# Kernel tuning notes

Hardware: AMD Instinct MI355X
Metric: run time of the kernel (lower is better)

Reference implementation:

```python
import jax, jax.numpy as jnp
import numpy as np

VOCAB = 1_000_000
EMBED = 128
NUM_NEG = 64
BATCH = 16384


def setup_inputs() -> dict:
    key = jax.random.key(0)
    k1, k2, k3, k4, k5, k6 = jax.random.split(key, 6)
    target = jax.random.randint(k1, (BATCH, 1), 0, VOCAB, dtype=jnp.int64 if jax.config.jax_enable_x64 else jnp.int32).astype(jnp.int32)
    context = jax.random.randint(k2, (BATCH, 1), 0, VOCAB).astype(jnp.int32)
    negatives = jax.random.randint(k3, (BATCH, NUM_NEG), 0, VOCAB).astype(jnp.int32)
    emb_table = jax.random.normal(k4, (VOCAB, EMBED), dtype=jnp.float32)
    w_table = jax.random.normal(k5, (VOCAB, EMBED), dtype=jnp.float32)
    b_table = jax.random.normal(k6, (VOCAB, 1), dtype=jnp.float32)
    return {
        "target": target,
        "context": context,
        "negatives": negatives,
        "emb_table": emb_table,
        "w_table": w_table,
        "b_table": b_table,
    }


def reference(target, context, negatives, emb_table, w_table, b_table):
    # context embedding: [B, 1, E]
    embed = emb_table[context]  # gather, [B, 1, E]
    # samples = concat(target, negatives): [B, 1 + NUM_NEG]
    samples = jnp.concatenate([target, negatives], axis=1)
    softmax_w = w_table[samples]          # [B, S, E]
    softmax_b = b_table[samples][..., 0]  # [B, S]
    # Dot(axes=2): [B,1,E] x [B,S,E] -> [B,S] logits (squeezing the 1)
    logits = jnp.einsum("boe,bse->bs", embed, softmax_w) + softmax_b
    return jax.nn.softmax(logits, axis=-1)  # [B, 1+NUM_NEG]
```

## Files before the change

### kernel.cpp

```cpp
#include <hip/hip_runtime.h>

#define BATCH   16384
#define NUM_NEG 64
#define NSAMP   65
#define EMBED   128

__global__ __launch_bounds__(256)
void skipgram_kernel(const int* __restrict__ target,
                     const int* __restrict__ context,
                     const int* __restrict__ negatives,
                     const float* __restrict__ emb_table,
                     const float* __restrict__ w_table,
                     const float* __restrict__ b_table,
                     float* __restrict__ out)
{
    const int b    = blockIdx.x;
    const int tid  = threadIdx.x;
    const int wave = tid >> 6;
    const int half = (tid >> 5) & 1;
    const int l32  = tid & 31;
    const int lane = tid & 63;

    __shared__ int   s_idx[NSAMP];
    __shared__ float s_logit[NSAMP];

    if (tid < NSAMP)
        s_idx[tid] = (tid == 0) ? target[b] : negatives[b * NUM_NEG + (tid - 1)];
    __syncthreads();

    const int c = context[b];
    const float4 e4 = *reinterpret_cast<const float4*>(
        &emb_table[(size_t)c * EMBED + 4 * l32]);

    float4 w4[8];
    float  bias[8];
    #pragma unroll
    for (int i = 0; i < 8; ++i) {
        const int s   = 8 * i + 2 * wave + half;
        const int idx = s_idx[s];
        w4[i]   = *reinterpret_cast<const float4*>(
                      &w_table[(size_t)idx * EMBED + 4 * l32]);
        bias[i] = b_table[idx];
    }

    #pragma unroll
    for (int i = 0; i < 8; ++i) {
        const int s = 8 * i + 2 * wave + half;
        float p = e4.x * w4[i].x + e4.y * w4[i].y
                + e4.z * w4[i].z + e4.w * w4[i].w;
        #pragma unroll
        for (int off = 16; off; off >>= 1)
            p += __shfl_xor(p, off, 32);
        if (l32 == 0)
            s_logit[s] = p + bias[i];
    }

    if (wave == 1 && half == 0) {
        const int idx = s_idx[64];
        const float4 v = *reinterpret_cast<const float4*>(
            &w_table[(size_t)idx * EMBED + 4 * l32]);
        const float bb = b_table[idx];
        float p = e4.x * v.x + e4.y * v.y + e4.z * v.z + e4.w * v.w;
        #pragma unroll
        for (int off = 16; off; off >>= 1)
            p += __shfl_xor(p, off, 32);
        if (l32 == 0)
            s_logit[64] = p + bb;
    }
    __syncthreads();

    if (wave == 0) {
        const float x  = s_logit[lane];
        const float x2 = (lane == 0) ? s_logit[64] : -INFINITY;

        float m = fmaxf(x, x2);
        #pragma unroll
        for (int off = 32; off; off >>= 1)
            m = fmaxf(m, __shfl_xor(m, off, 64));

        const float p  = __expf(x - m);
        const float p2 = (lane == 0) ? __expf(x2 - m) : 0.0f;

        float sum = p + p2;
        #pragma unroll
        for (int off = 32; off; off >>= 1)
            sum += __shfl_xor(sum, off, 64);

        const float inv = 1.0f / sum;
        out[(size_t)b * NSAMP + lane] = p * inv;
        if (lane == 0)
            out[(size_t)b * NSAMP + 64] = p2 * inv;
    }
}

extern "C" void kernel_launch(void* const* d_in, const int* in_sizes, int n_in,
                              void* d_out, int out_size, void* d_ws, size_t ws_size,
                              hipStream_t stream)
{
    const int*   target    = (const int*)  d_in[0];
    const int*   context   = (const int*)  d_in[1];
    const int*   negatives = (const int*)  d_in[2];
    const float* emb_table = (const float*)d_in[3];
    const float* w_table   = (const float*)d_in[4];
    const float* b_table   = (const float*)d_in[5];
    float*       out       = (float*)      d_out;

    skipgram_kernel<<<BATCH, 256, 0, stream>>>(
        target, context, negatives, emb_table, w_table, b_table, out);
}
```

Measured before the change: 100.2 us.

## Sort gathered sample indices by vocab row via counting sort before dot products

Replaces the single fused per-batch kernel with a pipeline of nine kernels. They histogram the sampled w_table indices, prefix-scan the counts and scatter (index, slot) pairs so that lookups of the same vocab row become adjacent. The context embeddings are first copied into a dense workspace buffer, and a separate softmax pass normalizes each row. The goal is better locality for the random w_table gathers. The cost is many extra launches, global atomics, extra reads of ctx and pairs, and a second pass over the output, while with 1M vocab and about 1M samples there is little row reuse to gain.

```diff
diff --git a/kernel.cpp b/kernel.cpp
--- a/kernel.cpp
+++ b/kernel.cpp
@@ -4,15 +4,182 @@
 #define NUM_NEG 64
 #define NSAMP   65
 #define EMBED   128
-
-__global__ __launch_bounds__(256)
-void skipgram_kernel(const int* __restrict__ target,
-                     const int* __restrict__ context,
-                     const int* __restrict__ negatives,
-                     const float* __restrict__ emb_table,
-                     const float* __restrict__ w_table,
-                     const float* __restrict__ b_table,
-                     float* __restrict__ out)
+#define VOCAB   1000000
+#define NPAIRS  (BATCH * NSAMP)
+#define SCAN_ELEMS 1024
+#define SCAN_NBLK  977
+
+#define OFF_PART  4194304
+#define OFF_PAIRS 4259840
+#define OFF_CTX   12779520
+#define WS_NEED   21168128
+
+
+__global__ __launch_bounds__(256)
+void k_zero(unsigned int* __restrict__ hist)
+{
+    hist[blockIdx.x * 256 + threadIdx.x] = 0u;
+}
+
+__global__ __launch_bounds__(256)
+void k_hist(const int* __restrict__ target, const int* __restrict__ negatives,
+            unsigned int* __restrict__ hist)
+{
+    const int t = blockIdx.x * 256 + threadIdx.x;
+    const int b = t / NSAMP, s = t - b * NSAMP;
+    const int idx = (s == 0) ? target[b] : negatives[b * NUM_NEG + (s - 1)];
+    atomicAdd(&hist[idx], 1u);
+}
+
+__global__ __launch_bounds__(256)
+void k_scan_local(unsigned int* __restrict__ hist, unsigned int* __restrict__ partials)
+{
+    __shared__ unsigned int lds[256];
+    const int base = blockIdx.x * SCAN_ELEMS + threadIdx.x * 4;
+    unsigned int v[4], s = 0;
+    #pragma unroll
+    for (int j = 0; j < 4; ++j) {
+        const unsigned int x = (base + j < VOCAB) ? hist[base + j] : 0u;
+        v[j] = x; s += x;
+    }
+    lds[threadIdx.x] = s;
+    __syncthreads();
+    for (int off = 1; off < 256; off <<= 1) {
+        const unsigned int t = (threadIdx.x >= off) ? lds[threadIdx.x - off] : 0u;
+        __syncthreads();
+        lds[threadIdx.x] += t;
+        __syncthreads();
+    }
+    if (threadIdx.x == 255) partials[blockIdx.x] = lds[255];
+    unsigned int run = lds[threadIdx.x] - s;
+    #pragma unroll
+    for (int j = 0; j < 4; ++j) {
+        const unsigned int x = v[j];
+        if (base + j < VOCAB) hist[base + j] = run;
+        run += x;
+    }
+}
+
+__global__ __launch_bounds__(1024)
+void k_scan_part(unsigned int* __restrict__ partials, int n)
+{
+    __shared__ unsigned int lds[1024];
+    const int t = threadIdx.x;
+    const unsigned int x = (t < n) ? partials[t] : 0u;
+    lds[t] = x;
+    __syncthreads();
+    for (int off = 1; off < 1024; off <<= 1) {
+        const unsigned int v = (t >= off) ? lds[t - off] : 0u;
+        __syncthreads();
+        lds[t] += v;
+        __syncthreads();
+    }
+    if (t < n) partials[t] = lds[t] - x;
+}
+
+__global__ __launch_bounds__(256)
+void k_addback(unsigned int* __restrict__ hist, const unsigned int* __restrict__ partials)
+{
+    const int base = blockIdx.x * SCAN_ELEMS + threadIdx.x * 4;
+    const unsigned int add = partials[blockIdx.x];
+    #pragma unroll
+    for (int j = 0; j < 4; ++j)
+        if (base + j < VOCAB) hist[base + j] += add;
+}
+
+__global__ __launch_bounds__(256)
+void k_scatter(const int* __restrict__ target, const int* __restrict__ negatives,
+               unsigned int* __restrict__ off, unsigned long long* __restrict__ pairs)
+{
+    const int t = blockIdx.x * 256 + threadIdx.x;
+    const int b = t / NSAMP, s = t - b * NSAMP;
+    const int idx = (s == 0) ? target[b] : negatives[b * NUM_NEG + (s - 1)];
+    const unsigned int pos = atomicAdd(&off[idx], 1u);
+    pairs[pos] = ((unsigned long long)(unsigned int)idx << 32)
+               | (unsigned int)(b * NSAMP + s);
+}
+
+__global__ __launch_bounds__(256)
+void k_densify(const int* __restrict__ context, const float* __restrict__ emb_table,
+               float* __restrict__ ctx)
+{
+    const int b = blockIdx.x * 2 + (threadIdx.x >> 7);
+    const int e = threadIdx.x & 127;
+    const int c = context[b];
+    ctx[(size_t)b * EMBED + e] = emb_table[(size_t)c * EMBED + e];
+}
+
+__global__ __launch_bounds__(256)
+void k_dot(const unsigned long long* __restrict__ pairs,
+           const float* __restrict__ w_table, const float* __restrict__ b_table,
+           const float* __restrict__ ctx, float* __restrict__ out)
+{
+    const int l32  = threadIdx.x & 31;
+    const int base = (blockIdx.x * 8 + (threadIdx.x >> 5)) * 8;
+
+    float4 wv[8], cv[8];
+    float  bias[8];
+    int    slot[8];
+    #pragma unroll
+    for (int i = 0; i < 8; ++i) {
+        const unsigned long long pr = pairs[base + i];
+        const int idx = (int)(pr >> 32);
+        slot[i] = (int)(pr & 0xffffffffu);
+        wv[i]   = *reinterpret_cast<const float4*>(
+                      &w_table[(size_t)idx * EMBED + 4 * l32]);
+        bias[i] = b_table[idx];
+        const int b = slot[i] / NSAMP;
+        cv[i]   = *reinterpret_cast<const float4*>(
+                      &ctx[(size_t)b * EMBED + 4 * l32]);
+    }
+    #pragma unroll
+    for (int i = 0; i < 8; ++i) {
+        float p = wv[i].x * cv[i].x + wv[i].y * cv[i].y
+                + wv[i].z * cv[i].z + wv[i].w * cv[i].w;
+        #pragma unroll
+        for (int off = 16; off; off >>= 1)
+            p += __shfl_xor(p, off, 32);
+        if (l32 == 0)
+            out[slot[i]] = p + bias[i];
+    }
+}
+
+__global__ __launch_bounds__(256)
+void k_softmax(float* __restrict__ out)
+{
+    const int lane = threadIdx.x & 63;
+    const int r    = blockIdx.x * 4 + (threadIdx.x >> 6);
+    float* row = out + (size_t)r * NSAMP;
+
+    const float x  = row[lane];
+    const float x2 = (lane == 0) ? row[64] : -INFINITY;
+
+    float m = fmaxf(x, x2);
+    #pragma unroll
+    for (int off = 32; off; off >>= 1)
+        m = fmaxf(m, __shfl_xor(m, off, 64));
+
+    const float p  = __expf(x - m);
+    const float p2 = (lane == 0) ? __expf(x2 - m) : 0.0f;
+
+    float sum = p + p2;
+    #pragma unroll
+    for (int off = 32; off; off >>= 1)
+        sum += __shfl_xor(sum, off, 64);
+
+    const float inv = 1.0f / sum;
+    row[lane] = p * inv;
+    if (lane == 0) row[64] = p2 * inv;
+}
+
+__global__ __launch_bounds__(256)
+void skipgram_fallback(const int* __restrict__ target,
+                       const int* __restrict__ context,
+                       const int* __restrict__ negatives,
+                       const float* __restrict__ emb_table,
+                       const float* __restrict__ w_table,
+                       const float* __restrict__ b_table,
+                       float* __restrict__ out)
 {
     const int b    = blockIdx.x;
     const int tid  = threadIdx.x;
@@ -42,7 +209,6 @@
                       &w_table[(size_t)idx * EMBED + 4 * l32]);
         bias[i] = b_table[idx];
     }
-
     #pragma unroll
     for (int i = 0; i < 8; ++i) {
         const int s = 8 * i + 2 * wave + half;
@@ -54,7 +220,6 @@
         if (l32 == 0)
             s_logit[s] = p + bias[i];
     }
-
     if (wave == 1 && half == 0) {
         const int idx = s_idx[64];
         const float4 v = *reinterpret_cast<const float4*>(
@@ -72,20 +237,16 @@
     if (wave == 0) {
         const float x  = s_logit[lane];
         const float x2 = (lane == 0) ? s_logit[64] : -INFINITY;
-
         float m = fmaxf(x, x2);
         #pragma unroll
         for (int off = 32; off; off >>= 1)
             m = fmaxf(m, __shfl_xor(m, off, 64));
-
         const float p  = __expf(x - m);
         const float p2 = (lane == 0) ? __expf(x2 - m) : 0.0f;
-
         float sum = p + p2;
         #pragma unroll
         for (int off = 32; off; off >>= 1)
             sum += __shfl_xor(sum, off, 64);
-
         const float inv = 1.0f / sum;
         out[(size_t)b * NSAMP + lane] = p * inv;
         if (lane == 0)
@@ -105,6 +266,25 @@
     const float* b_table   = (const float*)d_in[5];
     float*       out       = (float*)      d_out;
 
-    skipgram_kernel<<<BATCH, 256, 0, stream>>>(
-        target, context, negatives, emb_table, w_table, b_table, out);
-}
+    if (ws_size < (size_t)WS_NEED) {
+        skipgram_fallback<<<BATCH, 256, 0, stream>>>(
+            target, context, negatives, emb_table, w_table, b_table, out);
+        return;
+    }
+
+    char* ws = (char*)d_ws;
+    unsigned int*       hist     = (unsigned int*)       ws;
+    unsigned int*       partials = (unsigned int*)      (ws + OFF_PART);
+    unsigned long long* pairs    = (unsigned long long*)(ws + OFF_PAIRS);
+    float*              ctx      = (float*)             (ws + OFF_CTX);
+
+    k_zero     <<<4096,      256,  0, stream>>>(hist);
+    k_hist     <<<4160,      256,  0, stream>>>(target, negatives, hist);
+    k_scan_local<<<SCAN_NBLK,256,  0, stream>>>(hist, partials);
+    k_scan_part<<<1,         1024, 0, stream>>>(partials, SCAN_NBLK);
+    k_addback  <<<SCAN_NBLK, 256,  0, stream>>>(hist, partials);
+    k_scatter  <<<4160,      256,  0, stream>>>(target, negatives, hist, pairs);
+    k_densify  <<<8192,      256,  0, stream>>>(context, emb_table, ctx);
+    k_dot      <<<16640,     256,  0, stream>>>(pairs, w_table, b_table, ctx, out);
+    k_softmax  <<<4096,      256,  0, stream>>>(out);
+}
```

New measurement: 283.4 us. 2.83x slower.
